# Performance work log

Measured on AMD Instinct MI355X. Metric: run time of the kernel, lower is better.

## Reference

```python
import jax, jax.numpy as jnp
import numpy as np

B, S, H, D = 4, 2048, 16, 128
E = H * D  # emb_dim = 2048


def setup_inputs() -> dict:
    key = jax.random.key(0)
    ks = jax.random.split(key, 9)
    s_in = 1.0 / np.sqrt(E)
    return {
        "inputs": jax.random.normal(ks[0], (B, S, E), dtype=jnp.float32),
        "Wq": jax.random.normal(ks[1], (E, E), dtype=jnp.float32) * s_in,
        "bq": jnp.zeros((E,), dtype=jnp.float32),
        "Wk": jax.random.normal(ks[2], (E, E), dtype=jnp.float32) * s_in,
        "bk": jnp.zeros((E,), dtype=jnp.float32),
        "Wv": jax.random.normal(ks[3], (E, E), dtype=jnp.float32) * s_in,
        "bv": jnp.zeros((E,), dtype=jnp.float32),
        "Wo": jax.random.normal(ks[4], (E, E), dtype=jnp.float32) * s_in,
        "bo": jnp.zeros((E,), dtype=jnp.float32),
    }


def reference(inputs, Wq, bq, Wk, bk, Wv, bv, Wo, bo):
    b, s, e = inputs.shape
    # QKV projections -> [B, H, S, D]
    q = (inputs @ Wq + bq).reshape(b, s, H, D).transpose(0, 2, 1, 3)
    k = (inputs @ Wk + bk).reshape(b, s, H, D).transpose(0, 2, 1, 3)
    v = (inputs @ Wv + bv).reshape(b, s, H, D).transpose(0, 2, 1, 3)
    scale = 1.0 / jnp.sqrt(jnp.asarray(D, dtype=q.dtype))
    # Scaled dot-product attention (what the blockwise flash loop computes)
    scores = jnp.einsum('bhqd,bhkd->bhqk', q, k) * scale
    probs = jax.nn.softmax(scores, axis=-1)
    attn = jnp.einsum('bhqk,bhkd->bhqd', probs, v)
    attn = attn.transpose(0, 2, 1, 3).reshape(b, s, e)
    return attn @ Wo + bo
```

## Files before the change

### kernel.cpp

```cpp
#include <hip/hip_runtime.h>
#include <hip/hip_bf16.h>
#include <stdint.h>

typedef __bf16 bf16;
typedef float f32x4 __attribute__((ext_vector_type(4)));
typedef bf16 bf16x4 __attribute__((ext_vector_type(4)));
typedef bf16 bf16x8 __attribute__((ext_vector_type(8)));

#define DEV __device__ __forceinline__

DEV void gload16(const void* g, void* l) {
  __builtin_amdgcn_global_load_lds((const __attribute__((address_space(1))) void*)g,
                                   (__attribute__((address_space(3))) void*)l, 16, 0, 0);
}

DEV f32x4 mfma16(bf16x8 a, bf16x8 b, f32x4 c) {
  return __builtin_amdgcn_mfma_f32_16x16x32_bf16(a, b, c, 0, 0, 0);
}

#if __has_builtin(__builtin_amdgcn_exp2f)
DEV float EXP2F(float x) { return __builtin_amdgcn_exp2f(x); }
#else
DEV float EXP2F(float x) { return exp2f(x); }
#endif

static constexpr int Bn = 4, Sn = 2048, Hn = 16, Dn = 128, En = 2048, Mn = 8192;

__global__ void cvt_x(const float* __restrict__ in, bf16* __restrict__ out, int n8) {
  int i = blockIdx.x * blockDim.x + threadIdx.x;
  int stride = gridDim.x * blockDim.x;
  for (int idx = i; idx < n8; idx += stride) {
    const float4* p = (const float4*)(in + (size_t)idx * 8);
    float4 a = p[0], b = p[1];
    bf16x8 o;
    o[0]=(bf16)a.x; o[1]=(bf16)a.y; o[2]=(bf16)a.z; o[3]=(bf16)a.w;
    o[4]=(bf16)b.x; o[5]=(bf16)b.y; o[6]=(bf16)b.z; o[7]=(bf16)b.w;
    *(bf16x8*)(out + (size_t)idx * 8) = o;
  }
}

__global__ void wtrans(const float* __restrict__ W, bf16* __restrict__ Wt) {
  __shared__ bf16 t[64][65];
  int tx = threadIdx.x & 15, ty = threadIdx.x >> 4;
  int c0 = blockIdx.x * 64, r0 = blockIdx.y * 64;
  #pragma unroll
  for (int i = 0; i < 4; ++i) {
    int r = i * 16 + ty;
    float4 v = *(const float4*)&W[(size_t)(r0 + r) * En + c0 + tx * 4];
    t[r][tx*4+0] = (bf16)v.x; t[r][tx*4+1] = (bf16)v.y;
    t[r][tx*4+2] = (bf16)v.z; t[r][tx*4+3] = (bf16)v.w;
  }
  __syncthreads();
  #pragma unroll
  for (int i = 0; i < 4; ++i) {
    int c = i * 16 + ty;
    bf16x4 o;
    #pragma unroll
    for (int j = 0; j < 4; ++j) o[j] = t[tx*4+j][c];
    *(bf16x4*)&Wt[(size_t)(c0 + c) * En + r0 + tx * 4] = o;
  }
}

#define STAGE_A(H, DBUF, KTN) do { \
    const bf16* s_ = A + (size_t)(mbase + (tid >> 2)) * K + (KTN) * 64 + (H) * 32 \
                     + (((tid & 3) ^ ((tid >> 3) & 3)) * 8); \
    uint8_t* d_ = (DBUF) + (H) * 16384 + (w << 10); \
    gload16(s_, d_); \
    gload16(s_ + (size_t)128 * K, d_ + 8192); \
  } while (0)
#define STAGE_B(H, DBUF, KTN) do { \
    const bf16* s_ = Bt + (size_t)(nbase + (tid >> 2)) * K + (KTN) * 64 + (H) * 32 \
                     + (((tid & 3) ^ ((tid >> 3) & 3)) * 8); \
    uint8_t* d_ = (DBUF) + (H) * 16384 + (w << 10); \
    gload16(s_, d_); \
    gload16(s_ + (size_t)128 * K, d_ + 8192); \
  } while (0)

template<int OUT_MODE>
__global__ __launch_bounds__(512, 2) void gemm256(
    const bf16* __restrict__ A, const bf16* __restrict__ Bt,
    const float* __restrict__ b0, const float* __restrict__ b1,
    const float* __restrict__ b2, void* __restrict__ Cout,
    bf16* __restrict__ Vout,
    int M, int N, int K, int nbx)
{
  __shared__ __align__(16) uint8_t smem[131072];
  const int tid = threadIdx.x, lane = tid & 63, w = tid >> 6;
  const int wm = w >> 2, wn = w & 3;
  const int g = lane >> 4, lr = lane & 15;
  const int gx = (g ^ ((lr >> 1) & 3)) << 4;
  const int lid = blockIdx.x;
  const int swz = (lid & 7) * ((int)gridDim.x >> 3) + (lid >> 3);
  const int bx = swz % nbx, by = swz / nbx;
  const int mbase = by * 256, nbase = bx * 256;

  f32x4 acc[8][4] = {};

  STAGE_A(0, smem, 0);
  STAGE_B(0, smem + 65536, 0);
  STAGE_A(1, smem, 0);
  STAGE_B(1, smem + 65536, 0);
  asm volatile("s_waitcnt vmcnt(4)" ::: "memory");
  __builtin_amdgcn_s_barrier();

  const int NKT = K >> 6;
  for (int kt = 0; kt < NKT; ++kt) {
    const int cur = kt & 1;
    uint8_t* Acur = smem + (cur << 15);
    uint8_t* Bcur = smem + 65536 + (cur << 15);
    uint8_t* Anxt = smem + ((cur ^ 1) << 15);
    uint8_t* Bnxt = smem + 65536 + ((cur ^ 1) << 15);
    const bool notlast = (kt + 1 < NKT);
    bf16x8 af[8], bfr0, bfr1;

    #pragma unroll
    for (int mf = 0; mf < 8; ++mf)
      af[mf] = *(const bf16x8*)(Acur + (wm * 128 + mf * 16 + lr) * 64 + gx);
    bfr0 = *(const bf16x8*)(Bcur + (wn * 64 +  0 + lr) * 64 + gx);
    bfr1 = *(const bf16x8*)(Bcur + (wn * 64 + 16 + lr) * 64 + gx);
    if (notlast) STAGE_A(0, Anxt, kt + 1);
    __builtin_amdgcn_s_barrier();
    asm volatile("s_waitcnt lgkmcnt(0)" ::: "memory");
    __builtin_amdgcn_sched_barrier(0);
    __builtin_amdgcn_s_setprio(1);
    #pragma unroll
    for (int mf = 0; mf < 8; ++mf) {
      acc[mf][0] = mfma16(af[mf], bfr0, acc[mf][0]);
      acc[mf][1] = mfma16(af[mf], bfr1, acc[mf][1]);
    }
    __builtin_amdgcn_s_setprio(0);
    __builtin_amdgcn_s_barrier();

    bfr0 = *(const bf16x8*)(Bcur + (wn * 64 + 32 + lr) * 64 + gx);
    bfr1 = *(const bf16x8*)(Bcur + (wn * 64 + 48 + lr) * 64 + gx);
    if (notlast) STAGE_B(0, Bnxt, kt + 1);
    __builtin_amdgcn_s_barrier();
    asm volatile("s_waitcnt lgkmcnt(0)" ::: "memory");
    __builtin_amdgcn_sched_barrier(0);
    __builtin_amdgcn_s_setprio(1);
    #pragma unroll
    for (int mf = 0; mf < 8; ++mf) {
      acc[mf][2] = mfma16(af[mf], bfr0, acc[mf][2]);
      acc[mf][3] = mfma16(af[mf], bfr1, acc[mf][3]);
    }
    __builtin_amdgcn_s_setprio(0);
    if (notlast) { asm volatile("s_waitcnt vmcnt(4)" ::: "memory"); }
    else         { asm volatile("s_waitcnt vmcnt(0)" ::: "memory"); }
    __builtin_amdgcn_s_barrier();

    #pragma unroll
    for (int mf = 0; mf < 8; ++mf)
      af[mf] = *(const bf16x8*)(Acur + 16384 + (wm * 128 + mf * 16 + lr) * 64 + gx);
    bfr0 = *(const bf16x8*)(Bcur + 16384 + (wn * 64 +  0 + lr) * 64 + gx);
    bfr1 = *(const bf16x8*)(Bcur + 16384 + (wn * 64 + 16 + lr) * 64 + gx);
    if (notlast) STAGE_A(1, Anxt, kt + 1);
    __builtin_amdgcn_s_barrier();
    asm volatile("s_waitcnt lgkmcnt(0)" ::: "memory");
    __builtin_amdgcn_sched_barrier(0);
    __builtin_amdgcn_s_setprio(1);
    #pragma unroll
    for (int mf = 0; mf < 8; ++mf) {
      acc[mf][0] = mfma16(af[mf], bfr0, acc[mf][0]);
      acc[mf][1] = mfma16(af[mf], bfr1, acc[mf][1]);
    }
    __builtin_amdgcn_s_setprio(0);
    __builtin_amdgcn_s_barrier();

    bfr0 = *(const bf16x8*)(Bcur + 16384 + (wn * 64 + 32 + lr) * 64 + gx);
    bfr1 = *(const bf16x8*)(Bcur + 16384 + (wn * 64 + 48 + lr) * 64 + gx);
    if (notlast) STAGE_B(1, Bnxt, kt + 1);
    __builtin_amdgcn_s_barrier();
    asm volatile("s_waitcnt lgkmcnt(0)" ::: "memory");
    __builtin_amdgcn_sched_barrier(0);
    __builtin_amdgcn_s_setprio(1);
    #pragma unroll
    for (int mf = 0; mf < 8; ++mf) {
      acc[mf][2] = mfma16(af[mf], bfr0, acc[mf][2]);
      acc[mf][3] = mfma16(af[mf], bfr1, acc[mf][3]);
    }
    __builtin_amdgcn_s_setprio(0);
    asm volatile("s_waitcnt vmcnt(4)" ::: "memory");
    __builtin_amdgcn_s_barrier();
  }

  if constexpr (OUT_MODE == 0) {
    int tsel = nbase >> 11;
    if (tsel == 2) {
      #pragma unroll
      for (int j = 0; j < 4; ++j) {
        int nn = (nbase + wn * 64 + j * 16 + lr) & 2047;
        int h = nn >> 7, d = nn & 127;
        float bv = b2[nn];
        #pragma unroll
        for (int mf = 0; mf < 8; ++mf) {
          int m0 = mbase + wm * 128 + mf * 16 + g * 4;
          int b = m0 >> 11, s0 = m0 & 2047;
          bf16x4 o4;
          #pragma unroll
          for (int r = 0; r < 4; ++r) o4[r] = (bf16)(acc[mf][j][r] + bv);
          *(bf16x4*)&Vout[((size_t)(b * Hn + h) * Dn + d) * Sn + s0] = o4;
        }
      }
    } else {
      const float* bsel = (tsel == 0) ? b0 : b1;
      #pragma unroll
      for (int j = 0; j < 4; ++j) {
        int n = nbase + wn * 64 + j * 16 + lr;
        int nn = n & 2047;
        float bv = bsel[nn];
        int h = nn >> 7, d = nn & 127;
        #pragma unroll
        for (int mf = 0; mf < 8; ++mf) {
          #pragma unroll
          for (int r = 0; r < 4; ++r) {
            int m = mbase + wm * 128 + mf * 16 + g * 4 + r;
            int b = m >> 11, s = m & 2047;
            ((bf16*)Cout)[(size_t)tsel * ((size_t)Mn * En) +
                          ((size_t)(b * Hn + h) * Sn + s) * Dn + d] = (bf16)(acc[mf][j][r] + bv);
          }
        }
      }
    }
  } else {
    #pragma unroll
    for (int j = 0; j < 4; ++j) {
      int n = nbase + wn * 64 + j * 16 + lr;
      float bv = b0[n];
      #pragma unroll
      for (int mf = 0; mf < 8; ++mf) {
        #pragma unroll
        for (int r = 0; r < 4; ++r) {
          int m = mbase + wm * 128 + mf * 16 + g * 4 + r;
          ((float*)Cout)[(size_t)m * N + n] = acc[mf][j][r] + bv;
        }
      }
    }
  }
}

__global__ __launch_bounds__(512, 2) void attn(
    const bf16* __restrict__ Q, const bf16* __restrict__ K,
    const bf16* __restrict__ Vt, bf16* __restrict__ O)
{
  __shared__ __align__(16) uint8_t smem[65536];
  const int tid = threadIdx.x, lane = tid & 63, w = tid >> 6;
  const int g = lane >> 4, lr = lane & 15;
  const int lid = blockIdx.x;
  const int xcd = lid & 7, j = lid >> 3;
  const int bh = xcd * 8 + (j >> 3);
  const int q0 = (j & 7) * 256;
  const size_t hoff = (size_t)bh * Sn * Dn;
  const bf16* Qh = Q + hoff;
  const bf16* Kh = K + hoff;
  const bf16* Vh = Vt + hoff;
  const float SC2 = 0.12751744f;

  #pragma unroll
  for (int it = 0; it < 8; ++it) {
    int cl = it * 512 + tid;
    int row = cl >> 4, cs = cl & 15;
    int cg = cs ^ (row & 7);
    gload16(Qh + (size_t)(q0 + row) * Dn + cg * 8, smem + (it * 512 + (tid & ~63)) * 16);
  }
  __syncthreads();
  bf16x8 qf[2][4];
  #pragma unroll
  for (int nf = 0; nf < 2; ++nf)
    #pragma unroll
    for (int ks = 0; ks < 4; ++ks) {
      int row = w * 32 + nf * 16 + lr;
      qf[nf][ks] = *(const bf16x8*)(smem + row * 256 + (((ks * 4 + g) ^ (row & 7)) << 4));
    }
  __syncthreads();

  const int vd = tid >> 2, vq = tid & 3;
  const bf16* vrow = Vh + (size_t)vd * Sn + (vq >> 1) * 32 + (vq & 1) * 8;

  uint4 u0, u1;
  #pragma unroll
  for (int it = 0; it < 2; ++it) {
    int cl = it * 512 + tid;
    int row = cl >> 4, cs = cl & 15;
    int cg = cs ^ (row & 7);
    gload16(Kh + (size_t)row * Dn + cg * 8, smem + (it * 512 + (tid & ~63)) * 16);
  }
  { const uint4* vs = (const uint4*)vrow; u0 = vs[0]; u1 = vs[2]; }

  f32x4 o[2][8] = {};
  float m2[2] = { -__builtin_inff(), -__builtin_inff() };
  float lrun[2] = { 0.f, 0.f };

  for (int t = 0; t < 32; ++t) {
    const int cur = t & 1;
    uint8_t* Kcur = smem + (cur << 14);
    uint8_t* Knxt = smem + ((cur ^ 1) << 14);
    uint8_t* Vcur = smem + 32768 + (cur << 14);
    asm volatile("s_waitcnt vmcnt(0)" ::: "memory");
    {
      uint8_t* base = Vcur + vd * 128;
      const int sw = vd & 7;
      *(uint4*)(base + (((2 * vq + 0) ^ sw) << 4)) = make_uint4(u0.x, u0.y, u1.x, u1.y);
      *(uint4*)(base + (((2 * vq + 1) ^ sw) << 4)) = make_uint4(u0.z, u0.w, u1.z, u1.w);
    }
    if (t < 31) {
      const int kvn = (t + 1) * 64;
      #pragma unroll
      for (int it = 0; it < 2; ++it) {
        int cl = it * 512 + tid;
        int row = cl >> 4, cs = cl & 15;
        int cg = cs ^ (row & 7);
        gload16(Kh + (size_t)(kvn + row) * Dn + cg * 8,
                Knxt + (it * 512 + (tid & ~63)) * 16);
      }
      const uint4* vs = (const uint4*)(vrow + kvn);
      u0 = vs[0]; u1 = vs[2];
    }
    asm volatile("s_waitcnt lgkmcnt(0)" ::: "memory");
    asm volatile("s_barrier" ::: "memory");

    f32x4 sfr[2][4] = {};
    __builtin_amdgcn_s_setprio(1);
    #pragma unroll
    for (int ks = 0; ks < 4; ++ks) {
      #pragma unroll
      for (int mf = 0; mf < 4; ++mf) {
        int row = mf * 16 + lr;
        bf16x8 kf = *(const bf16x8*)(Kcur + row * 256 + (((ks * 4 + g) ^ (row & 7)) << 4));
        sfr[0][mf] = mfma16(kf, qf[0][ks], sfr[0][mf]);
        sfr[1][mf] = mfma16(kf, qf[1][ks], sfr[1][mf]);
      }
    }
    __builtin_amdgcn_s_setprio(0);

    bf16x8 pa[2][2];
    #pragma unroll
    for (int nf = 0; nf < 2; ++nf) {
      f32x4 a0, a1;
      #pragma unroll
      for (int r = 0; r < 4; ++r) a0[r] = fmaxf(sfr[nf][0][r], sfr[nf][1][r]);
      #pragma unroll
      for (int r = 0; r < 4; ++r) a1[r] = fmaxf(sfr[nf][2][r], sfr[nf][3][r]);
      #pragma unroll
      for (int r = 0; r < 4; ++r) a0[r] = fmaxf(a0[r], a1[r]);
      float mx = fmaxf(fmaxf(a0[0], a0[1]), fmaxf(a0[2], a0[3]));
      mx = fmaxf(mx, __shfl_xor(mx, 16));
      mx = fmaxf(mx, __shfl_xor(mx, 32));
      float pm2 = mx * SC2;
      if (__any(pm2 > m2[nf] + 8.f)) {
        float mnew = fmaxf(m2[nf], pm2);
        float fsc = EXP2F(m2[nf] - mnew);
        m2[nf] = mnew;
        lrun[nf] *= fsc;
        float fv[4];
        #pragma unroll
        for (int r = 0; r < 4; ++r) fv[r] = __shfl(fsc, g * 4 + r);
        #pragma unroll
        for (int df = 0; df < 8; ++df)
          #pragma unroll
          for (int r = 0; r < 4; ++r) o[nf][df][r] *= fv[r];
      }
      const float mc = m2[nf];
      f32x4 p[4];
      #pragma unroll
      for (int mf = 0; mf < 4; ++mf)
        #pragma unroll
        for (int r = 0; r < 4; ++r)
          p[mf][r] = EXP2F(__builtin_fmaf(sfr[nf][mf][r], SC2, -mc));
      f32x4 s0, s1;
      #pragma unroll
      for (int r = 0; r < 4; ++r) s0[r] = p[0][r] + p[1][r];
      #pragma unroll
      for (int r = 0; r < 4; ++r) s1[r] = p[2][r] + p[3][r];
      #pragma unroll
      for (int r = 0; r < 4; ++r) s0[r] += s1[r];
      float ps = (s0[0] + s0[1]) + (s0[2] + s0[3]);
      ps += __shfl_xor(ps, 16);
      ps += __shfl_xor(ps, 32);
      lrun[nf] += ps;
      #pragma unroll
      for (int ks = 0; ks < 2; ++ks) {
        bf16x8 tt;
        #pragma unroll
        for (int i = 0; i < 4; ++i) {
          tt[i]     = (bf16)p[2 * ks][i];
          tt[i + 4] = (bf16)p[2 * ks + 1][i];
        }
        pa[nf][ks] = tt;
      }
    }

    __builtin_amdgcn_s_setprio(1);
    #pragma unroll
    for (int ks = 0; ks < 2; ++ks) {
      #pragma unroll
      for (int df = 0; df < 8; ++df) {
        int row = df * 16 + lr;
        bf16x8 vf = *(const bf16x8*)(Vcur + row * 128 + (((ks * 4 + g) ^ (row & 7)) << 4));
        o[0][df] = mfma16(pa[0][ks], vf, o[0][df]);
        o[1][df] = mfma16(pa[1][ks], vf, o[1][df]);
      }
    }
    __builtin_amdgcn_s_setprio(0);
    asm volatile("s_barrier" ::: "memory");
  }

  const int b = bh >> 4, h = bh & 15;
  #pragma unroll
  for (int nf = 0; nf < 2; ++nf) {
    float inv = 1.f / lrun[nf];
    float iv[4];
    #pragma unroll
    for (int r = 0; r < 4; ++r) iv[r] = __shfl(inv, g * 4 + r);
    #pragma unroll
    for (int df = 0; df < 8; ++df) {
      #pragma unroll
      for (int r = 0; r < 4; ++r) {
        int qrow = q0 + w * 32 + nf * 16 + g * 4 + r;
        int d = df * 16 + lr;
        size_t m = (size_t)b * Sn + qrow;
        O[m * En + h * Dn + d] = (bf16)(o[nf][df][r] * iv[r]);
      }
    }
  }
}

extern "C" void kernel_launch(void* const* d_in, const int* in_sizes, int n_in,
                              void* d_out, int out_size, void* d_ws, size_t ws_size,
                              hipStream_t stream) {
  const float* X  = (const float*)d_in[0];
  const float* Wq = (const float*)d_in[1];
  const float* bq = (const float*)d_in[2];
  const float* Wk = (const float*)d_in[3];
  const float* bk = (const float*)d_in[4];
  const float* Wv = (const float*)d_in[5];
  const float* bv = (const float*)d_in[6];
  const float* Wo = (const float*)d_in[7];
  const float* bo = (const float*)d_in[8];

  bf16* ws = (bf16*)d_ws;
  const size_t szE = (size_t)Mn * En;
  const size_t szW = (size_t)En * En;
  bf16* Xb  = ws;
  bf16* Wqt = Xb + szE;
  bf16* Wkt = Wqt + szW;
  bf16* Wvt = Wkt + szW;
  bf16* Wot = Wvt + szW;
  bf16* Qb  = Wot + szW;
  bf16* Kb  = Qb + szE;
  bf16* Vb  = Kb + szE;
  bf16* Vtp = Vb + szE;
  bf16* AO  = Vb;

  cvt_x<<<2048, 256, 0, stream>>>(X, Xb, (int)(szE / 8));
  wtrans<<<dim3(32, 32), 256, 0, stream>>>(Wq, Wqt);
  wtrans<<<dim3(32, 32), 256, 0, stream>>>(Wk, Wkt);
  wtrans<<<dim3(32, 32), 256, 0, stream>>>(Wv, Wvt);
  wtrans<<<dim3(32, 32), 256, 0, stream>>>(Wo, Wot);
  gemm256<0><<<768, 512, 0, stream>>>(Xb, Wqt, bq, bk, bv, Qb, Vtp, Mn, 3 * En, En, 24);
  attn<<<512, 512, 0, stream>>>(Qb, Kb, Vtp, AO);
  gemm256<1><<<256, 512, 0, stream>>>(AO, Wot, bo, nullptr, nullptr, d_out, nullptr, Mn, En, En, 8);
}
```

Measured before the change: 479.3 us.

## Simplify GEMM main loop to issue full next-tile prefetch upfront with one barrier

```diff
diff --git a/kernel.cpp b/kernel.cpp
--- a/kernel.cpp
+++ b/kernel.cpp
@@ -100,7 +100,7 @@
   STAGE_B(0, smem + 65536, 0);
   STAGE_A(1, smem, 0);
   STAGE_B(1, smem + 65536, 0);
-  asm volatile("s_waitcnt vmcnt(4)" ::: "memory");
+  asm volatile("s_waitcnt vmcnt(0)" ::: "memory");
   __builtin_amdgcn_s_barrier();
 
   const int NKT = K >> 6;
@@ -111,75 +111,42 @@
     uint8_t* Anxt = smem + ((cur ^ 1) << 15);
     uint8_t* Bnxt = smem + 65536 + ((cur ^ 1) << 15);
     const bool notlast = (kt + 1 < NKT);
-    bf16x8 af[8], bfr0, bfr1;
-
+
+    if (notlast) {
+      STAGE_A(0, Anxt, kt + 1);
+      STAGE_B(0, Bnxt, kt + 1);
+      STAGE_A(1, Anxt, kt + 1);
+      STAGE_B(1, Bnxt, kt + 1);
+    }
+
+    bf16x8 a0[8], b0v[4], a1[8], b1v[4];
     #pragma unroll
     for (int mf = 0; mf < 8; ++mf)
-      af[mf] = *(const bf16x8*)(Acur + (wm * 128 + mf * 16 + lr) * 64 + gx);
-    bfr0 = *(const bf16x8*)(Bcur + (wn * 64 +  0 + lr) * 64 + gx);
-    bfr1 = *(const bf16x8*)(Bcur + (wn * 64 + 16 + lr) * 64 + gx);
-    if (notlast) STAGE_A(0, Anxt, kt + 1);
-    __builtin_amdgcn_s_barrier();
-    asm volatile("s_waitcnt lgkmcnt(0)" ::: "memory");
-    __builtin_amdgcn_sched_barrier(0);
+      a0[mf] = *(const bf16x8*)(Acur + (wm * 128 + mf * 16 + lr) * 64 + gx);
+    #pragma unroll
+    for (int j = 0; j < 4; ++j)
+      b0v[j] = *(const bf16x8*)(Bcur + (wn * 64 + j * 16 + lr) * 64 + gx);
+    #pragma unroll
+    for (int mf = 0; mf < 8; ++mf)
+      a1[mf] = *(const bf16x8*)(Acur + 16384 + (wm * 128 + mf * 16 + lr) * 64 + gx);
+    #pragma unroll
+    for (int j = 0; j < 4; ++j)
+      b1v[j] = *(const bf16x8*)(Bcur + 16384 + (wn * 64 + j * 16 + lr) * 64 + gx);
+
     __builtin_amdgcn_s_setprio(1);
     #pragma unroll
-    for (int mf = 0; mf < 8; ++mf) {
-      acc[mf][0] = mfma16(af[mf], bfr0, acc[mf][0]);
-      acc[mf][1] = mfma16(af[mf], bfr1, acc[mf][1]);
-    }
+    for (int mf = 0; mf < 8; ++mf)
+      #pragma unroll
+      for (int j = 0; j < 4; ++j)
+        acc[mf][j] = mfma16(a0[mf], b0v[j], acc[mf][j]);
+    #pragma unroll
+    for (int mf = 0; mf < 8; ++mf)
+      #pragma unroll
+      for (int j = 0; j < 4; ++j)
+        acc[mf][j] = mfma16(a1[mf], b1v[j], acc[mf][j]);
     __builtin_amdgcn_s_setprio(0);
-    __builtin_amdgcn_s_barrier();
-
-    bfr0 = *(const bf16x8*)(Bcur + (wn * 64 + 32 + lr) * 64 + gx);
-    bfr1 = *(const bf16x8*)(Bcur + (wn * 64 + 48 + lr) * 64 + gx);
-    if (notlast) STAGE_B(0, Bnxt, kt + 1);
-    __builtin_amdgcn_s_barrier();
-    asm volatile("s_waitcnt lgkmcnt(0)" ::: "memory");
-    __builtin_amdgcn_sched_barrier(0);
-    __builtin_amdgcn_s_setprio(1);
-    #pragma unroll
-    for (int mf = 0; mf < 8; ++mf) {
-      acc[mf][2] = mfma16(af[mf], bfr0, acc[mf][2]);
-      acc[mf][3] = mfma16(af[mf], bfr1, acc[mf][3]);
-    }
-    __builtin_amdgcn_s_setprio(0);
-    if (notlast) { asm volatile("s_waitcnt vmcnt(4)" ::: "memory"); }
-    else         { asm volatile("s_waitcnt vmcnt(0)" ::: "memory"); }
-    __builtin_amdgcn_s_barrier();
-
-    #pragma unroll
-    for (int mf = 0; mf < 8; ++mf)
-      af[mf] = *(const bf16x8*)(Acur + 16384 + (wm * 128 + mf * 16 + lr) * 64 + gx);
-    bfr0 = *(const bf16x8*)(Bcur + 16384 + (wn * 64 +  0 + lr) * 64 + gx);
-    bfr1 = *(const bf16x8*)(Bcur + 16384 + (wn * 64 + 16 + lr) * 64 + gx);
-    if (notlast) STAGE_A(1, Anxt, kt + 1);
-    __builtin_amdgcn_s_barrier();
-    asm volatile("s_waitcnt lgkmcnt(0)" ::: "memory");
-    __builtin_amdgcn_sched_barrier(0);
-    __builtin_amdgcn_s_setprio(1);
-    #pragma unroll
-    for (int mf = 0; mf < 8; ++mf) {
-      acc[mf][0] = mfma16(af[mf], bfr0, acc[mf][0]);
-      acc[mf][1] = mfma16(af[mf], bfr1, acc[mf][1]);
-    }
-    __builtin_amdgcn_s_setprio(0);
-    __builtin_amdgcn_s_barrier();
-
-    bfr0 = *(const bf16x8*)(Bcur + 16384 + (wn * 64 + 32 + lr) * 64 + gx);
-    bfr1 = *(const bf16x8*)(Bcur + 16384 + (wn * 64 + 48 + lr) * 64 + gx);
-    if (notlast) STAGE_B(1, Bnxt, kt + 1);
-    __builtin_amdgcn_s_barrier();
-    asm volatile("s_waitcnt lgkmcnt(0)" ::: "memory");
-    __builtin_amdgcn_sched_barrier(0);
-    __builtin_amdgcn_s_setprio(1);
-    #pragma unroll
-    for (int mf = 0; mf < 8; ++mf) {
-      acc[mf][2] = mfma16(af[mf], bfr0, acc[mf][2]);
-      acc[mf][3] = mfma16(af[mf], bfr1, acc[mf][3]);
-    }
-    __builtin_amdgcn_s_setprio(0);
-    asm volatile("s_waitcnt vmcnt(4)" ::: "memory");
+
+    asm volatile("s_waitcnt vmcnt(0)" ::: "memory");
     __builtin_amdgcn_s_barrier();
   }
 
```

Result: no change. 475.8 us (-0.7%).
